# Optimization experiments

Measured on AMD Instinct MI355X. Metric: run time of the kernel, lower is better.

## Reference

```python
import math
import jax, jax.numpy as jnp
import numpy as np

# ---- static configuration (matches init_kwargs) ----
NM, NT, NF = 250000, 8000, 60000      # movable, terminals(fixed), filler
N = NM + NT + NF
XL = YL = ZL = 0.0
XH, YH, ZH = 512.0, 512.0, 8.0
BSX = BSY = BSZ = 1.0
NX = int(round((XH - XL) / BSX))
NY = int(round((YH - YL) / BSY))
NZ = int(round((ZH - ZL) / BSZ))
TD = 1.0                              # target density
PAD = 1
SQRT2 = 1.4142135623730951
BIN_VOL = BSX * BSY * BSZ


def _padding_mask():
    m = np.ones((NX, NY, NZ), dtype=bool)
    m[PAD:NX - PAD, PAD:NY - PAD, PAD:NZ - PAD] = False
    return jnp.asarray(m)


def _axis_overlap(p0, s, bl, bs, K, NB):
    """Overlap of segment [p0, p0+s] with K consecutive bins starting at floor bin.
    Returns bin indices [n,K], overlap lengths [n,K], validity mask [n,K]."""
    i0 = jnp.floor((p0 - bl) / bs).astype(jnp.int32)               # [n]
    k = i0[:, None] + jnp.arange(K, dtype=jnp.int32)               # [n,K]
    lo = bl + k.astype(p0.dtype) * bs                              # bin left edges
    ov = jnp.clip(jnp.minimum(p0[:, None] + s[:, None], lo + bs)
                  - jnp.maximum(p0[:, None], lo), 0.0)
    valid = (k >= 0) & (k < NB)
    return jnp.clip(k, 0, NB - 1), ov, valid


def _scatter_density(grid_flat, x0, y0, z0, sx, sy, sz, w, Kx, Ky, Kz):
    """Overlap-weighted scatter-add of boxes into the flat [NX*NY*NZ] density map."""
    kx, ox, vx = _axis_overlap(x0, sx, XL, BSX, Kx, NX)
    ky, oy, vy = _axis_overlap(y0, sy, YL, BSY, Ky, NY)
    kz, oz, vz = _axis_overlap(z0, sz, ZL, BSZ, Kz, NZ)
    val = (w[:, None, None, None]
           * ox[:, :, None, None] * oy[:, None, :, None] * oz[:, None, None, :])
    valid = vx[:, :, None, None] & vy[:, None, :, None] & vz[:, None, None, :]
    val = jnp.where(valid, val, 0.0)
    idx = (kx[:, :, None, None] * NY + ky[:, None, :, None]) * NZ + kz[:, None, None, :]
    return grid_flat.at[idx.reshape(-1)].add(val.reshape(-1))


def setup_inputs() -> dict:
    key = jax.random.key(0)
    k1, k2, k3, k4, k5, k6 = jax.random.split(key, 6)
    node_size_x = jax.random.uniform(k1, (N,), jnp.float32, 0.5, 1.0)
    node_size_y = jax.random.uniform(k2, (N,), jnp.float32, 0.5, 1.0)
    node_size_z = jax.random.uniform(k3, (N,), jnp.float32, 0.5, 1.0)
    px = jax.random.uniform(k4, (N,), jnp.float32, XL, XH - 1.0)
    py = jax.random.uniform(k5, (N,), jnp.float32, YL, YH - 1.0)
    pz = jax.random.uniform(k6, (N,), jnp.float32, ZL, ZH - 1.0)
    pos = jnp.concatenate([px, py, pz])  # flat x|y|z layout as in pos.view(numel)
    bin_center_x = XL + (jnp.arange(NX, dtype=jnp.float32) + 0.5) * BSX
    bin_center_y = YL + (jnp.arange(NY, dtype=jnp.float32) + 0.5) * BSY
    bin_center_z = ZL + (jnp.arange(NZ, dtype=jnp.float32) + 0.5) * BSZ
    sorted_node_map = jnp.arange(NM, dtype=jnp.int32)
    return {"pos": pos, "node_size_x": node_size_x, "node_size_y": node_size_y,
            "node_size_z": node_size_z, "bin_center_x": bin_center_x,
            "bin_center_y": bin_center_y, "bin_center_z": bin_center_z,
            "sorted_node_map": sorted_node_map}


def reference(pos, node_size_x, node_size_y, node_size_z,
              bin_center_x, bin_center_y, bin_center_z, sorted_node_map):
    px, py, pz = pos[:N], pos[N:2 * N], pos[2 * N:]

    # reset(): stretched (clamped) sizes, offsets, area-preserving ratio
    csx = jnp.maximum(node_size_x, BSX * SQRT2)
    csy = jnp.maximum(node_size_y, BSY * SQRT2)
    csz = jnp.maximum(node_size_z, BSZ * SQRT2)
    offx = (node_size_x - csx) * 0.5
    offy = (node_size_y - csy) * 0.5
    offz = (node_size_z - csz) * 0.5
    ratio = (node_size_x * node_size_y * node_size_z) / (csx * csy * csz)

    # ---- initial density map from fixed cells (terminals), actual sizes ----
    f0, f1 = NM, NM + NT
    Kfx = int(min(NX, math.ceil((float(jnp.max(node_size_x[f0:f1])) + BSX) / BSX)))
    Kfy = int(min(NY, math.ceil((float(jnp.max(node_size_y[f0:f1])) + BSY) / BSY)))
    Kfz = int(min(NZ, math.ceil((float(jnp.max(node_size_z[f0:f1])) + BSZ) / BSZ)))
    grid = jnp.zeros(NX * NY * NZ, dtype=jnp.float32)
    grid = _scatter_density(grid, px[f0:f1], py[f0:f1], pz[f0:f1],
                            node_size_x[f0:f1], node_size_y[f0:f1], node_size_z[f0:f1],
                            jnp.ones((NT,), jnp.float32), Kfx, Kfy, Kfz)
    grid = grid * TD  # initial_density_map.mul_(target_density)

    # ---- movable + filler cells: stretched sizes, offset, ratio weight ----
    mf = jnp.concatenate([jnp.arange(NM), jnp.arange(N - NF, N)])
    Kx = int(min(NX, math.ceil((float(jnp.max(node_size_x[mf])) + 2 * SQRT2 * BSX) / BSX)))
    Ky = int(min(NY, math.ceil((float(jnp.max(node_size_y[mf])) + 2 * SQRT2 * BSY) / BSY)))
    Kz = int(min(NZ, math.ceil((float(jnp.max(node_size_z[mf])) + 2 * SQRT2 * BSZ) / BSZ)))
    grid = _scatter_density(grid,
                            px[mf] + offx[mf], py[mf] + offy[mf], pz[mf] + offz[mf],
                            csx[mf], csy[mf], csz[mf], ratio[mf], Kx, Ky, Kz)

    density_map = grid.reshape(NX, NY, NZ)
    density_map = jnp.where(_padding_mask(), TD * BIN_VOL, density_map)

    density_cost = jnp.maximum(density_map - TD * BIN_VOL, 0.0).sum()[None]
    max_density = (density_map.max() / BIN_VOL)[None]
    return density_cost, max_density
```

## Files before the change

### kernel.cpp

```cpp
#include <hip/hip_runtime.h>

#define NMOV 250000
#define NTRM 8000
#define NTOT 318000
#define GNX 512
#define GNY 512
#define GNZ 8
#define TSX 16
#define TSY 16
#define NTX 32
#define NTY 32
#define NTILES 1024
#define NSH 16
#define CAPS 96
#define SMAX 768

static __device__ __forceinline__ float axis_ov(float p0, float s, int k) {
    float lo = (float)k;
    return fmaxf(fminf(p0 + s, lo + 1.0f) - fmaxf(p0, lo), 0.0f);
}
static __device__ __forceinline__ float ovz(float pz, float pzh, int k) {
    float lo = (float)k;
    return fmaxf(fminf(pzh, lo + 1.0f) - fmaxf(pz, lo), 0.0f);
}

static __device__ __forceinline__ void node_box(
    int i, const float* __restrict__ pos,
    const float* __restrict__ nsx, const float* __restrict__ nsy, const float* __restrict__ nsz,
    float& px, float& py, float& pz, float& ex, float& ey, float& ez, float& w)
{
    px = pos[i]; py = pos[NTOT + i]; pz = pos[2 * NTOT + i];
    float sx = nsx[i], sy = nsy[i], sz = nsz[i];
    const float S2 = 1.4142135623730951f;
    bool terminal = (i >= NMOV) && (i < NMOV + NTRM);
    if (!terminal) {
        float cx = fmaxf(sx, S2), cy = fmaxf(sy, S2), cz = fmaxf(sz, S2);
        px += (sx - cx) * 0.5f;
        py += (sy - cy) * 0.5f;
        pz += (sz - cz) * 0.5f;
        w = (sx * sy * sz) / (cx * cy * cz);
        ex = cx; ey = cy; ez = cz;
    } else {
        ex = sx; ey = sy; ez = sz; w = 1.0f;
    }
}

__global__ void fill_kernel(const float* __restrict__ pos,
                            const float* __restrict__ nsx,
                            const float* __restrict__ nsy,
                            const float* __restrict__ nsz,
                            int* __restrict__ counts,
                            int* __restrict__ bucket,
                            float4* __restrict__ pA,
                            float4* __restrict__ pB,
                            int write_params) {
    int i = blockIdx.x * blockDim.x + threadIdx.x;
    if (i >= NTOT) return;
    float px, py, pz, ex, ey, ez, w;
    node_box(i, pos, nsx, nsy, nsz, px, py, pz, ex, ey, ez, w);

    if (write_params) {
        pA[i] = make_float4(px, px + ex, py, py + ey);
        pB[i] = make_float4(pz, pz + ez, w, 0.0f);
    }

    int ix0 = max((int)floorf(px), 0);
    int ix1 = min((int)floorf(px + ex), GNX - 1);
    int iy0 = max((int)floorf(py), 0);
    int iy1 = min((int)floorf(py + ey), GNY - 1);
    int tx0 = ix0 >> 4, tx1 = ix1 >> 4;
    int ty0 = iy0 >> 4, ty1 = iy1 >> 4;
    int s = i & (NSH - 1);
    for (int tx = tx0; tx <= tx1; ++tx) {
        for (int ty = ty0; ty <= ty1; ++ty) {
            int cell = (tx * NTY + ty) * NSH + s;
            int idx = atomicAdd(&counts[cell], 1);
            if (idx < CAPS) bucket[cell * CAPS + idx] = i;
        }
    }
}

__launch_bounds__(256)
__global__ void accum_fast_kernel(const int* __restrict__ counts,
                                  const int* __restrict__ bucket,
                                  const float4* __restrict__ pA,
                                  const float4* __restrict__ pB,
                                  float* __restrict__ out) {
    __shared__ float4 sQ[SMAX];
    __shared__ float4 sWA[SMAX];
    __shared__ float4 sWB[SMAX];
    __shared__ int offs[NSH + 1];

    int t = blockIdx.x;
    int tx = t >> 5, ty = t & (NTY - 1);
    int x = (tx << 4) + (threadIdx.x >> 4);
    int y = (ty << 4) + (threadIdx.x & 15);
    float Xf = (float)x, Yf = (float)y;

    float acc[GNZ];
    #pragma unroll
    for (int z = 0; z < GNZ; ++z) acc[z] = 0.0f;

    if (threadIdx.x == 0) {
        int run = 0; offs[0] = 0;
        #pragma unroll
        for (int s = 0; s < NSH; ++s) {
            run += min(counts[t * NSH + s], CAPS);
            offs[s + 1] = run;
        }
    }
    __syncthreads();
    int tot = offs[NSH];

    for (int base = 0; base < tot; base += SMAX) {
        int m = min(tot - base, SMAX);
        for (int f = threadIdx.x; f < m; f += 256) {
            int g = base + f;
            int s = 0;
            while (offs[s + 1] <= g) ++s;
            int idx = g - offs[s];
            int id = bucket[(t * NSH + s) * CAPS + idx];
            float4 q = pA[id];
            float4 r = pB[id];
            sQ[f] = q;
            float pz = r.x, pzh = r.y, w = r.z;
            sWA[f] = make_float4(w * ovz(pz, pzh, 0), w * ovz(pz, pzh, 1),
                                 w * ovz(pz, pzh, 2), w * ovz(pz, pzh, 3));
            sWB[f] = make_float4(w * ovz(pz, pzh, 4), w * ovz(pz, pzh, 5),
                                 w * ovz(pz, pzh, 6), w * ovz(pz, pzh, 7));
        }
        __syncthreads();
        for (int j = 0; j < m; ++j) {
            float4 q = sQ[j];
            float ox = fmaxf(fminf(q.y, Xf + 1.0f) - fmaxf(q.x, Xf), 0.0f);
            float oy = fmaxf(fminf(q.w, Yf + 1.0f) - fmaxf(q.z, Yf), 0.0f);
            float oxy = ox * oy;
            if (oxy > 0.0f) {
                float4 a = sWA[j];
                float4 b = sWB[j];
                acc[0] = fmaf(oxy, a.x, acc[0]);
                acc[1] = fmaf(oxy, a.y, acc[1]);
                acc[2] = fmaf(oxy, a.z, acc[2]);
                acc[3] = fmaf(oxy, a.w, acc[3]);
                acc[4] = fmaf(oxy, b.x, acc[4]);
                acc[5] = fmaf(oxy, b.y, acc[5]);
                acc[6] = fmaf(oxy, b.z, acc[6]);
                acc[7] = fmaf(oxy, b.w, acc[7]);
            }
        }
        __syncthreads();
    }

    float cost = 0.0f;
    float mx = 1.0f;
    if (x >= 1 && x <= GNX - 2 && y >= 1 && y <= GNY - 2) {
        #pragma unroll
        for (int z = 1; z <= GNZ - 2; ++z) {
            cost += fmaxf(acc[z] - 1.0f, 0.0f);
            mx = fmaxf(mx, acc[z]);
        }
    }
    #pragma unroll
    for (int off = 32; off >= 1; off >>= 1) {
        cost += __shfl_down(cost, off);
        mx = fmaxf(mx, __shfl_down(mx, off));
    }
    __shared__ float scost[4];
    __shared__ float smx[4];
    int lane = threadIdx.x & 63;
    int wid = threadIdx.x >> 6;
    if (lane == 0) { scost[wid] = cost; smx[wid] = mx; }
    __syncthreads();
    if (threadIdx.x == 0) {
        float c = scost[0] + scost[1] + scost[2] + scost[3];
        float m = fmaxf(fmaxf(smx[0], smx[1]), fmaxf(smx[2], smx[3]));
        atomicAdd(&out[0], c);
        atomicMax((int*)&out[1], __float_as_int(m));
    }
}

__launch_bounds__(256)
__global__ void accum_slow_kernel(const float* __restrict__ pos,
                                  const float* __restrict__ nsx,
                                  const float* __restrict__ nsy,
                                  const float* __restrict__ nsz,
                                  const int* __restrict__ counts,
                                  const int* __restrict__ bucket,
                                  float* __restrict__ out) {
    __shared__ float spx[CAPS], spxh[CAPS], spy[CAPS], spyh[CAPS];
    __shared__ float swoz[GNZ][CAPS];
    int t = blockIdx.x;
    int tx = t >> 5, ty = t & (NTY - 1);
    int x = (tx << 4) + (threadIdx.x >> 4);
    int y = (ty << 4) + (threadIdx.x & 15);
    float Xf = (float)x, Yf = (float)y;
    float acc[GNZ];
    #pragma unroll
    for (int z = 0; z < GNZ; ++z) acc[z] = 0.0f;
    for (int s = 0; s < NSH; ++s) {
        int cell = t * NSH + s;
        int n = min(counts[cell], CAPS);
        if ((int)threadIdx.x < n) {
            int i = bucket[cell * CAPS + threadIdx.x];
            float px, py, pz, ex, ey, ez, w;
            node_box(i, pos, nsx, nsy, nsz, px, py, pz, ex, ey, ez, w);
            spx[threadIdx.x] = px;  spxh[threadIdx.x] = px + ex;
            spy[threadIdx.x] = py;  spyh[threadIdx.x] = py + ey;
            #pragma unroll
            for (int z = 0; z < GNZ; ++z)
                swoz[z][threadIdx.x] = w * axis_ov(pz, ez, z);
        }
        __syncthreads();
        for (int j = 0; j < n; ++j) {
            float ox = fmaxf(fminf(spxh[j], Xf + 1.0f) - fmaxf(spx[j], Xf), 0.0f);
            float oy = fmaxf(fminf(spyh[j], Yf + 1.0f) - fmaxf(spy[j], Yf), 0.0f);
            float oxy = ox * oy;
            if (oxy > 0.0f) {
                #pragma unroll
                for (int z = 0; z < GNZ; ++z)
                    acc[z] = fmaf(oxy, swoz[z][j], acc[z]);
            }
        }
        __syncthreads();
    }
    float cost = 0.0f;
    float mx = 1.0f;
    if (x >= 1 && x <= GNX - 2 && y >= 1 && y <= GNY - 2) {
        #pragma unroll
        for (int z = 1; z <= GNZ - 2; ++z) {
            cost += fmaxf(acc[z] - 1.0f, 0.0f);
            mx = fmaxf(mx, acc[z]);
        }
    }
    #pragma unroll
    for (int off = 32; off >= 1; off >>= 1) {
        cost += __shfl_down(cost, off);
        mx = fmaxf(mx, __shfl_down(mx, off));
    }
    __shared__ float scost[4];
    __shared__ float smx[4];
    int lane = threadIdx.x & 63;
    int wid = threadIdx.x >> 6;
    if (lane == 0) { scost[wid] = cost; smx[wid] = mx; }
    __syncthreads();
    if (threadIdx.x == 0) {
        float c = scost[0] + scost[1] + scost[2] + scost[3];
        float m = fmaxf(fmaxf(smx[0], smx[1]), fmaxf(smx[2], smx[3]));
        atomicAdd(&out[0], c);
        atomicMax((int*)&out[1], __float_as_int(m));
    }
}

extern "C" void kernel_launch(void* const* d_in, const int* in_sizes, int n_in,
                              void* d_out, int out_size, void* d_ws, size_t ws_size,
                              hipStream_t stream) {
    const float* pos = (const float*)d_in[0];
    const float* nsx = (const float*)d_in[1];
    const float* nsy = (const float*)d_in[2];
    const float* nsz = (const float*)d_in[3];

    const size_t OFF_BUCKET = 65536;
    const size_t OFF_PA = 6356992;
    const size_t OFF_PB = 11444992;
    const size_t NEED = 16532992;

    int* counts = (int*)d_ws;
    int* bucket = (int*)((char*)d_ws + OFF_BUCKET);
    float4* pA = (float4*)((char*)d_ws + OFF_PA);
    float4* pB = (float4*)((char*)d_ws + OFF_PB);
    float* out = (float*)d_out;
    int fast = (ws_size >= NEED) ? 1 : 0;

    hipMemsetAsync(counts, 0, NTILES * NSH * sizeof(int), stream);
    hipMemsetAsync(out, 0, 2 * sizeof(float), stream);

    fill_kernel<<<(NTOT + 255) / 256, 256, 0, stream>>>(
        pos, nsx, nsy, nsz, counts, bucket, pA, pB, fast);
    if (fast) {
        accum_fast_kernel<<<NTILES, 256, 0, stream>>>(counts, bucket, pA, pB, out);
    } else {
        accum_slow_kernel<<<NTILES, 256, 0, stream>>>(pos, nsx, nsy, nsz, counts, bucket, out);
    }
}
```

Baseline: 160.6 us.

## Bin cells into 8x8 tiles with inline parameters, one wavefront per tile

```diff
diff --git a/kernel.cpp b/kernel.cpp
--- a/kernel.cpp
+++ b/kernel.cpp
@@ -6,14 +6,6 @@
 #define GNX 512
 #define GNY 512
 #define GNZ 8
-#define TSX 16
-#define TSY 16
-#define NTX 32
-#define NTY 32
-#define NTILES 1024
-#define NSH 16
-#define CAPS 96
-#define SMAX 768
 
 static __device__ __forceinline__ float axis_ov(float p0, float s, int k) {
     float lo = (float)k;
@@ -23,7 +15,6 @@
     float lo = (float)k;
     return fmaxf(fminf(pzh, lo + 1.0f) - fmaxf(pz, lo), 0.0f);
 }
-
 static __device__ __forceinline__ void node_box(
     int i, const float* __restrict__ pos,
     const float* __restrict__ nsx, const float* __restrict__ nsy, const float* __restrict__ nsz,
@@ -45,6 +36,127 @@
     }
 }
 
+#define NTX8 64
+#define NTY8 64
+#define NTIL8 4096
+#define CAP8 176
+
+__global__ void fill8_kernel(const float* __restrict__ pos,
+                             const float* __restrict__ nsx,
+                             const float* __restrict__ nsy,
+                             const float* __restrict__ nsz,
+                             int* __restrict__ counts,
+                             float4* __restrict__ bucket,
+                             float* __restrict__ out) {
+    int i = blockIdx.x * blockDim.x + threadIdx.x;
+    if (i == 0) { out[0] = 0.0f; out[1] = 0.0f; }
+    if (i >= NTOT) return;
+
+    float pxl, pyl, pzl, ex, ey, ez, w;
+    node_box(i, pos, nsx, nsy, nsz, pxl, pyl, pzl, ex, ey, ez, w);
+    float pxh = pxl + ex, pyh = pyl + ey, pzh = pzl + ez;
+
+    float4 q = make_float4(pxl, pxh, pyl, pyh);
+    float4 a = make_float4(w * ovz(pzl, pzh, 0), w * ovz(pzl, pzh, 1),
+                           w * ovz(pzl, pzh, 2), w * ovz(pzl, pzh, 3));
+    float4 b = make_float4(w * ovz(pzl, pzh, 4), w * ovz(pzl, pzh, 5),
+                           w * ovz(pzl, pzh, 6), w * ovz(pzl, pzh, 7));
+    float4 pad = make_float4(0.0f, 0.0f, 0.0f, 0.0f);
+
+    int ix0 = max((int)floorf(pxl), 0);
+    int ix1 = min((int)floorf(pxh), GNX - 1);
+    int iy0 = max((int)floorf(pyl), 0);
+    int iy1 = min((int)floorf(pyh), GNY - 1);
+    int tx0 = ix0 >> 3, tx1 = ix1 >> 3;
+    int ty0 = iy0 >> 3, ty1 = iy1 >> 3;
+
+    for (int tx = tx0; tx <= tx1; ++tx) {
+        for (int ty = ty0; ty <= ty1; ++ty) {
+            int cell = (tx << 6) + ty;
+            int idx = atomicAdd(&counts[cell], 1);
+            if (idx < CAP8) {
+                float4* s = bucket + ((size_t)(cell * CAP8 + idx) << 2);
+                s[0] = q; s[1] = a; s[2] = b; s[3] = pad;
+            }
+        }
+    }
+}
+
+__launch_bounds__(256)
+__global__ void accum8_kernel(const int* __restrict__ counts,
+                              const float4* __restrict__ bucket,
+                              float* __restrict__ out) {
+    __shared__ float4 seg[4][CAP8 * 3];
+    __shared__ float scost[4], smx[4];
+
+    int wid = threadIdx.x >> 6;
+    int lane = threadIdx.x & 63;
+    int t = (blockIdx.x << 2) + wid;
+    int tx = t >> 6, ty = t & 63;
+    int x = (tx << 3) + (lane >> 3);
+    int y = (ty << 3) + (lane & 7);
+    float Xf = (float)x, Yf = (float)y;
+
+    float acc[GNZ];
+    #pragma unroll
+    for (int z = 0; z < GNZ; ++z) acc[z] = 0.0f;
+
+    int n = min(counts[t], CAP8);
+    const float4* slot = bucket + ((size_t)t * CAP8 << 2);
+
+    for (int e = lane; e < n; e += 64) {
+        const float4* sp = slot + (e << 2);
+        seg[wid][e * 3 + 0] = sp[0];
+        seg[wid][e * 3 + 1] = sp[1];
+        seg[wid][e * 3 + 2] = sp[2];
+    }
+
+    for (int j = 0; j < n; ++j) {
+        float4 q = seg[wid][3 * j];
+        float ox = fmaxf(fminf(q.y, Xf + 1.0f) - fmaxf(q.x, Xf), 0.0f);
+        float oy = fmaxf(fminf(q.w, Yf + 1.0f) - fmaxf(q.z, Yf), 0.0f);
+        float oxy = ox * oy;
+        float4 a = seg[wid][3 * j + 1];
+        float4 b = seg[wid][3 * j + 2];
+        acc[0] = fmaf(oxy, a.x, acc[0]);
+        acc[1] = fmaf(oxy, a.y, acc[1]);
+        acc[2] = fmaf(oxy, a.z, acc[2]);
+        acc[3] = fmaf(oxy, a.w, acc[3]);
+        acc[4] = fmaf(oxy, b.x, acc[4]);
+        acc[5] = fmaf(oxy, b.y, acc[5]);
+        acc[6] = fmaf(oxy, b.z, acc[6]);
+        acc[7] = fmaf(oxy, b.w, acc[7]);
+    }
+
+    float cost = 0.0f;
+    float mx = 1.0f;
+    if (x >= 1 && x <= GNX - 2 && y >= 1 && y <= GNY - 2) {
+        #pragma unroll
+        for (int z = 1; z <= GNZ - 2; ++z) {
+            cost += fmaxf(acc[z] - 1.0f, 0.0f);
+            mx = fmaxf(mx, acc[z]);
+        }
+    }
+    #pragma unroll
+    for (int off = 32; off >= 1; off >>= 1) {
+        cost += __shfl_down(cost, off);
+        mx = fmaxf(mx, __shfl_down(mx, off));
+    }
+    if (lane == 0) { scost[wid] = cost; smx[wid] = mx; }
+    __syncthreads();
+    if (threadIdx.x == 0) {
+        float c = scost[0] + scost[1] + scost[2] + scost[3];
+        float m = fmaxf(fmaxf(smx[0], smx[1]), fmaxf(smx[2], smx[3]));
+        atomicAdd(&out[0], c);
+        atomicMax((int*)&out[1], __float_as_int(m));
+    }
+}
+
+#define NTY 32
+#define NSH 16
+#define CAPS 96
+#define SMAX 768
+
 __global__ void fill_kernel(const float* __restrict__ pos,
                             const float* __restrict__ nsx,
                             const float* __restrict__ nsy,
@@ -58,12 +170,10 @@
     if (i >= NTOT) return;
     float px, py, pz, ex, ey, ez, w;
     node_box(i, pos, nsx, nsy, nsz, px, py, pz, ex, ey, ez, w);
-
     if (write_params) {
         pA[i] = make_float4(px, px + ex, py, py + ey);
         pB[i] = make_float4(pz, pz + ez, w, 0.0f);
     }
-
     int ix0 = max((int)floorf(px), 0);
     int ix1 = min((int)floorf(px + ex), GNX - 1);
     int iy0 = max((int)floorf(py), 0);
@@ -90,17 +200,14 @@
     __shared__ float4 sWA[SMAX];
     __shared__ float4 sWB[SMAX];
     __shared__ int offs[NSH + 1];
-
     int t = blockIdx.x;
     int tx = t >> 5, ty = t & (NTY - 1);
     int x = (tx << 4) + (threadIdx.x >> 4);
     int y = (ty << 4) + (threadIdx.x & 15);
     float Xf = (float)x, Yf = (float)y;
-
     float acc[GNZ];
     #pragma unroll
     for (int z = 0; z < GNZ; ++z) acc[z] = 0.0f;
-
     if (threadIdx.x == 0) {
         int run = 0; offs[0] = 0;
         #pragma unroll
@@ -111,7 +218,6 @@
     }
     __syncthreads();
     int tot = offs[NSH];
-
     for (int base = 0; base < tot; base += SMAX) {
         int m = min(tot - base, SMAX);
         for (int f = threadIdx.x; f < m; f += 256) {
@@ -150,7 +256,6 @@
         }
         __syncthreads();
     }
-
     float cost = 0.0f;
     float mx = 1.0f;
     if (x >= 1 && x <= GNX - 2 && y >= 1 && y <= GNY - 2) {
@@ -258,27 +363,39 @@
     const float* nsx = (const float*)d_in[1];
     const float* nsy = (const float*)d_in[2];
     const float* nsz = (const float*)d_in[3];
-
+    float* out = (float*)d_out;
+
+    const size_t NEED8 = 65536 + (size_t)NTIL8 * CAP8 * 64;
     const size_t OFF_BUCKET = 65536;
     const size_t OFF_PA = 6356992;
     const size_t OFF_PB = 11444992;
-    const size_t NEED = 16532992;
-
-    int* counts = (int*)d_ws;
-    int* bucket = (int*)((char*)d_ws + OFF_BUCKET);
-    float4* pA = (float4*)((char*)d_ws + OFF_PA);
-    float4* pB = (float4*)((char*)d_ws + OFF_PB);
-    float* out = (float*)d_out;
-    int fast = (ws_size >= NEED) ? 1 : 0;
-
-    hipMemsetAsync(counts, 0, NTILES * NSH * sizeof(int), stream);
-    hipMemsetAsync(out, 0, 2 * sizeof(float), stream);
-
-    fill_kernel<<<(NTOT + 255) / 256, 256, 0, stream>>>(
-        pos, nsx, nsy, nsz, counts, bucket, pA, pB, fast);
-    if (fast) {
-        accum_fast_kernel<<<NTILES, 256, 0, stream>>>(counts, bucket, pA, pB, out);
+    const size_t NEED7 = 16532992;
+
+    if (ws_size >= NEED8) {
+        int* counts = (int*)d_ws;
+        float4* bucket = (float4*)((char*)d_ws + 65536);
+        hipMemsetAsync(counts, 0, NTIL8 * sizeof(int), stream);
+        fill8_kernel<<<(NTOT + 255) / 256, 256, 0, stream>>>(
+            pos, nsx, nsy, nsz, counts, bucket, out);
+        accum8_kernel<<<NTIL8 / 4, 256, 0, stream>>>(counts, bucket, out);
+    } else if (ws_size >= NEED7) {
+        int* counts = (int*)d_ws;
+        int* bucket = (int*)((char*)d_ws + OFF_BUCKET);
+        float4* pA = (float4*)((char*)d_ws + OFF_PA);
+        float4* pB = (float4*)((char*)d_ws + OFF_PB);
+        hipMemsetAsync(counts, 0, 1024 * NSH * sizeof(int), stream);
+        hipMemsetAsync(out, 0, 2 * sizeof(float), stream);
+        fill_kernel<<<(NTOT + 255) / 256, 256, 0, stream>>>(
+            pos, nsx, nsy, nsz, counts, bucket, pA, pB, 1);
+        accum_fast_kernel<<<1024, 256, 0, stream>>>(counts, bucket, pA, pB, out);
     } else {
-        accum_slow_kernel<<<NTILES, 256, 0, stream>>>(pos, nsx, nsy, nsz, counts, bucket, out);
-    }
-}
+        int* counts = (int*)d_ws;
+        int* bucket = (int*)((char*)d_ws + OFF_BUCKET);
+        hipMemsetAsync(counts, 0, 1024 * NSH * sizeof(int), stream);
+        hipMemsetAsync(out, 0, 2 * sizeof(float), stream);
+        fill_kernel<<<(NTOT + 255) / 256, 256, 0, stream>>>(
+            pos, nsx, nsy, nsz, counts, bucket, (float4*)nullptr, (float4*)nullptr, 0);
+        accum_slow_kernel<<<1024, 256, 0, stream>>>(
+            pos, nsx, nsy, nsz, counts, bucket, out);
+    }
+}
```

Measured after the change: 140.7 us. -12.4%, faster.
